# Kernel tuning notes

Hardware: AMD Instinct MI355X
Metric: run time of the kernel (lower is better)

The kernel has to match this reference:

```python
import jax, jax.numpy as jnp
import numpy as np
import math

C = 512
GROUPS = 32
EPS = 1e-06


def group_norm(x, w, b):
    # x: [B, C, H, W]; 32 groups over channels
    B, Cc, H, W = x.shape
    xg = x.reshape(B, GROUPS, Cc // GROUPS, H, W)
    mu = jnp.mean(xg, axis=(2, 3, 4), keepdims=True)
    var = jnp.var(xg, axis=(2, 3, 4), keepdims=True)
    xn = ((xg - mu) * jax.lax.rsqrt(var + EPS)).reshape(B, Cc, H, W)
    return xn * w[None, :, None, None] + b[None, :, None, None]


def setup_inputs() -> dict:
    key = jax.random.key(0)
    ks = jax.random.split(key, 7)
    B, H, W = 2, 64, 64
    x = jax.random.normal(ks[0], (B, C, H, W), dtype=jnp.float32)
    gn_w = jnp.ones((C,), dtype=jnp.float32)
    gn_b = jnp.zeros((C,), dtype=jnp.float32)
    s = 1.0 / math.sqrt(C)
    qkv_w = jax.random.normal(ks[1], (3 * C, C), dtype=jnp.float32) * s
    qkv_b = jnp.zeros((3 * C,), dtype=jnp.float32)
    proj_w = jax.random.normal(ks[2], (C, C), dtype=jnp.float32) * s
    proj_b = jnp.zeros((C,), dtype=jnp.float32)
    return {"x": x, "gn_w": gn_w, "gn_b": gn_b, "qkv_w": qkv_w,
            "qkv_b": qkv_b, "proj_w": proj_w, "proj_b": proj_b}


def reference(x, gn_w, gn_b, qkv_w, qkv_b, proj_w, proj_b):
    residue = x
    B, Cc, H, W = x.shape
    N = H * W
    constant = 1.0 / math.sqrt(Cc)
    xn = group_norm(x, gn_w, gn_b)
    # 1x1 conv == channel matmul
    qkv = jnp.einsum('bchw,oc->bohw', xn, qkv_w) + qkv_b[None, :, None, None]
    q, k, v = jnp.split(qkv, 3, axis=1)
    q = q.reshape(B, Cc, N)
    k = k.reshape(B, Cc, N)
    v = v.reshape(B, Cc, N)
    # attn[b,i,j] = sum_c k[b,c,i] * q[b,c,j]   (k^T @ q, per original code)
    attn = jnp.einsum('bci,bcj->bij', k, q) * constant
    soft = jax.nn.softmax(attn, axis=2)  # softmax over q-index j, as in torch dim=2
    # output[b,c,i] = sum_j v[b,c,j] * soft[b,j,i]   (v @ soft)
    out = jnp.einsum('bcj,bji->bci', v, soft).reshape(B, Cc, H, W)
    proj = jnp.einsum('bchw,oc->bohw', out, proj_w) + proj_b[None, :, None, None]
    return residue + proj
```

## Files before the change

kernel.cpp:

```cpp
#include <hip/hip_runtime.h>
#include <hip/hip_bf16.h>
#include <math.h>

typedef unsigned short ushort_t;
typedef __attribute__((ext_vector_type(8))) unsigned short ushort8;
typedef __attribute__((ext_vector_type(8))) __bf16 bf16x8;
typedef __attribute__((ext_vector_type(4))) float f32x4;

__device__ inline ushort_t f2b(float f) {
  __hip_bfloat16 h = __float2bfloat16(f);
  return __builtin_bit_cast(ushort_t, h);
}
__device__ inline float b2f(ushort_t u) {
  __hip_bfloat16 h = __builtin_bit_cast(__hip_bfloat16, u);
  return __bfloat162float(h);
}

__device__ inline void gload16(const ushort_t* g, ushort_t* l) {
  __builtin_amdgcn_global_load_lds(
      (const __attribute__((address_space(1))) unsigned int*)g,
      (__attribute__((address_space(3))) unsigned int*)l, 16, 0, 0);
}

__device__ inline void xcd_swz(int& bx, int& by, int& bz) {
  const int nx = gridDim.x, ny = gridDim.y;
  const int nwg = nx * ny * gridDim.z;
  const int orig = blockIdx.x + nx * (blockIdx.y + ny * blockIdx.z);
  const int q = nwg >> 3, r = nwg & 7, xcd = orig & 7, loc = orig >> 3;
  const int wg = (xcd < r ? xcd * (q + 1) : r * (q + 1) + (xcd - r) * q) + loc;
  bx = wg % nx;
  by = (wg / nx) % ny;
  bz = wg / (nx * ny);
}

__global__ __launch_bounds__(256) void prep_weights(
    const float* __restrict__ qkv_w, const float* __restrict__ proj_w,
    ushort_t* __restrict__ qkvw, ushort_t* __restrict__ projw) {
  int idx = blockIdx.x * 256 + threadIdx.x;
  const int NQ = 1536 * 512;
  if (idx < NQ) {
    qkvw[idx] = f2b(qkv_w[idx]);
  } else {
    int j = idx - NQ;
    if (j < 512 * 512) projw[j] = f2b(proj_w[j]);
  }
}

__global__ __launch_bounds__(256) void gn_stats(const float* __restrict__ x,
                                                float* __restrict__ stats) {
  const int tid = threadIdx.x;
  const int bg = blockIdx.x;
  const float4* xv = (const float4*)(x + (size_t)bg * 65536);
  float s = 0.f, ss = 0.f;
  for (int i = tid; i < 16384; i += 256) {
    float4 v = xv[i];
    s += v.x + v.y + v.z + v.w;
    ss += v.x * v.x + v.y * v.y + v.z * v.z + v.w * v.w;
  }
  __shared__ float red[8];
  for (int off = 32; off > 0; off >>= 1) {
    s += __shfl_down(s, off);
    ss += __shfl_down(ss, off);
  }
  if ((tid & 63) == 0) { red[tid >> 6] = s; red[4 + (tid >> 6)] = ss; }
  __syncthreads();
  if (tid == 0) {
    float st = red[0] + red[1] + red[2] + red[3];
    float sst = red[4] + red[5] + red[6] + red[7];
    float mean = st * (1.f / 65536.f);
    float var = sst * (1.f / 65536.f) - mean * mean;
    stats[bg * 2] = mean;
    stats[bg * 2 + 1] = rsqrtf(var + 1e-6f);
  }
}

__global__ __launch_bounds__(256) void gn_apply_t(
    const float* __restrict__ x, const float* __restrict__ w,
    const float* __restrict__ bgn, const float* __restrict__ stats,
    ushort_t* __restrict__ xnT) {
  __shared__ ushort_t tile[64][68];
  const int b = blockIdx.z;
  const int p0 = blockIdx.x * 64, c0 = blockIdx.y * 64;
  const int tid = threadIdx.x;
  const float* xb = x + ((size_t)b * 512 + c0) * 4096 + p0;
  const int tc = tid >> 4, tp = (tid & 15) * 4;
#pragma unroll
  for (int pass = 0; pass < 4; ++pass) {
    int c = pass * 16 + tc;
    int cg = c0 + c;
    float mean = stats[(b * 32 + (cg >> 4)) * 2];
    float inv = stats[(b * 32 + (cg >> 4)) * 2 + 1];
    float wc = w[cg] * inv;
    float bc = bgn[cg] - mean * wc;
    float4 v = *(const float4*)(xb + (size_t)c * 4096 + tp);
    tile[c][tp] = f2b(v.x * wc + bc);
    tile[c][tp + 1] = f2b(v.y * wc + bc);
    tile[c][tp + 2] = f2b(v.z * wc + bc);
    tile[c][tp + 3] = f2b(v.w * wc + bc);
  }
  __syncthreads();
  const int c8 = (tid & 7) * 8;
#pragma unroll
  for (int pass = 0; pass < 2; ++pass) {
    int p = pass * 32 + (tid >> 3);
    ushort8 u;
#pragma unroll
    for (int e = 0; e < 8; ++e) u[e] = tile[c8 + e][p];
    *(ushort8*)(xnT + ((size_t)b * 4096 + p0 + p) * 512 + c0 + c8) = u;
  }
}

template <int EPI>
__global__ __launch_bounds__(512, 2) void gemm8(
    const ushort_t* __restrict__ A, const ushort_t* __restrict__ B,
    void* __restrict__ Cg, const float* __restrict__ bias,
    float* __restrict__ smp, int N, int K, int lda, int ldb, size_t sA,
    size_t sB, size_t sC, float scale) {
  __shared__ __align__(16) ushort_t Al[2][256 * 64];
  __shared__ __align__(16) ushort_t Bl[2][256 * 64];
  __shared__ float s_max[2][256], s_sum[2][256];

  int bx, by, bz;
  xcd_swz(bx, by, bz);
  const ushort_t* Ab = A + bz * sA;
  const ushort_t* Bb = B + bz * sB;
  const int bm0 = by * 256, bn0 = bx * 256;
  const int tid = threadIdx.x;
  const int w = tid >> 6, lane = tid & 63;
  const int wr = w >> 2, wc = w & 3;
  const int fr = lane & 15, fq = lane >> 4;

  const int srow = tid >> 3, scb = tid & 7;
  const int ssw = scb ^ (srow & 7);
  const ushort_t* aS = Ab + (size_t)(bm0 + srow) * lda + ssw * 8;
  const ushort_t* bS = Bb + (size_t)(bn0 + srow) * ldb + ssw * 8;

  auto stage_a = [&](int s, int kk) {
#pragma unroll
    for (int g = 0; g < 4; ++g)
      gload16(aS + (size_t)(g * 64) * lda + kk, &Al[s][g * 4096 + w * 512]);
  };
  auto stage_b = [&](int s, int kk) {
#pragma unroll
    for (int g = 0; g < 4; ++g)
      gload16(bS + (size_t)(g * 64) * ldb + kk, &Bl[s][g * 4096 + w * 512]);
  };

  f32x4 acc[8][4] = {};
  bf16x8 a_r[4][2], b_r[4][2];

  auto read_a = [&](int s, int mh) {
#pragma unroll
    for (int mi = 0; mi < 4; ++mi) {
      int row = wr * 128 + mh * 64 + mi * 16 + fr;
#pragma unroll
      for (int ks = 0; ks < 2; ++ks) {
        int blk = ((ks * 4 + fq) ^ (row & 7)) * 8;
        a_r[mi][ks] = *(const bf16x8*)&Al[s][row * 64 + blk];
      }
    }
  };
  auto read_b = [&](int s, int nh) {
#pragma unroll
    for (int ni = 0; ni < 2; ++ni) {
      int row = wc * 64 + nh * 32 + ni * 16 + fr;
#pragma unroll
      for (int ks = 0; ks < 2; ++ks) {
        int blk = ((ks * 4 + fq) ^ (row & 7)) * 8;
        b_r[nh * 2 + ni][ks] = *(const bf16x8*)&Bl[s][row * 64 + blk];
      }
    }
  };
  auto phase_mfma = [&](int mh, int nh) {
    __builtin_amdgcn_s_setprio(1);
#pragma unroll
    for (int ks = 0; ks < 2; ++ks)
#pragma unroll
      for (int mi = 0; mi < 4; ++mi)
#pragma unroll
        for (int ni = 0; ni < 2; ++ni)
          acc[mh * 4 + mi][nh * 2 + ni] =
              __builtin_amdgcn_mfma_f32_16x16x32_bf16(
                  a_r[mi][ks], b_r[nh * 2 + ni][ks],
                  acc[mh * 4 + mi][nh * 2 + ni], 0, 0, 0);
    __builtin_amdgcn_s_setprio(0);
  };

  const int nt = K >> 6;
  stage_b(0, 0);
  stage_a(0, 0);
  if (nt > 1) {
    stage_b(1, 64);
    stage_a(1, 64);
    asm volatile("s_waitcnt vmcnt(8)" ::: "memory");
  } else {
    asm volatile("s_waitcnt vmcnt(0)" ::: "memory");
  }
  __builtin_amdgcn_s_barrier();

  for (int t = 0; t < nt; ++t) {
    const int s = t & 1;
    const int kk2 = (t + 2) << 6;
    const bool st2 = (t + 2) < nt;
    read_a(s, 0);
    read_b(s, 0);
    __builtin_amdgcn_s_barrier();
    phase_mfma(0, 0);
    __builtin_amdgcn_s_barrier();
    read_b(s, 1);
    __builtin_amdgcn_s_barrier();
    phase_mfma(0, 1);
    __builtin_amdgcn_s_barrier();
    read_a(s, 1);
    asm volatile("" ::: "memory");
    if (st2) stage_b(s, kk2);
    __builtin_amdgcn_s_barrier();
    phase_mfma(1, 0);
    __builtin_amdgcn_s_barrier();
    asm volatile("" ::: "memory");
    if (st2) stage_a(s, kk2);
    __builtin_amdgcn_s_barrier();
    phase_mfma(1, 1);
    if (st2)
      asm volatile("s_waitcnt vmcnt(8)" ::: "memory");
    else if (t + 1 < nt)
      asm volatile("s_waitcnt vmcnt(0)" ::: "memory");
    __builtin_amdgcn_s_barrier();
  }

  const size_t cbase = (size_t)bz * sC;
#pragma unroll
  for (int mi = 0; mi < 8; ++mi) {
#pragma unroll
    for (int r = 0; r < 4; ++r) {
      int gm = bm0 + wr * 128 + mi * 16 + fq * 4 + r;
#pragma unroll
      for (int ni = 0; ni < 4; ++ni) {
        int gn = bn0 + wc * 64 + ni * 16 + fr;
        float v = acc[mi][ni][r];
        size_t off = cbase + (size_t)gm * N + gn;
        ((ushort_t*)Cg)[off] = f2b(__expf(fminf(v * scale, 80.f)));
      }
    }
  }

  if constexpr (EPI == 2) {
    float cm[4], cs4[4];
#pragma unroll
    for (int ni = 0; ni < 4; ++ni) {
      float m = -3e38f;
#pragma unroll
      for (int mi = 0; mi < 8; ++mi)
#pragma unroll
        for (int r = 0; r < 4; ++r) m = fmaxf(m, acc[mi][ni][r] * scale);
      m = fmaxf(m, __shfl_xor(m, 16));
      m = fmaxf(m, __shfl_xor(m, 32));
      float s = 0.f;
#pragma unroll
      for (int mi = 0; mi < 8; ++mi)
#pragma unroll
        for (int r = 0; r < 4; ++r) s += __expf(acc[mi][ni][r] * scale - m);
      s += __shfl_xor(s, 16);
      s += __shfl_xor(s, 32);
      cm[ni] = m;
      cs4[ni] = s;
    }
    __syncthreads();
    if (lane < 16) {
#pragma unroll
      for (int ni = 0; ni < 4; ++ni) {
        s_max[wr][wc * 64 + ni * 16 + lane] = cm[ni];
        s_sum[wr][wc * 64 + ni * 16 + lane] = cs4[ni];
      }
    }
    __syncthreads();
    if (tid < 256) {
      float m0 = s_max[0][tid], m1 = s_max[1][tid];
      float M = fmaxf(m0, m1);
      float S = s_sum[0][tid] * __expf(m0 - M) + s_sum[1][tid] * __expf(m1 - M);
      size_t o = (((size_t)bz * 16 + by) * 4096 + bn0 + tid) * 2;
      smp[o] = M;
      smp[o + 1] = S;
    }
  }
}

template <int EPI>
__global__ __launch_bounds__(256) void gemm_pl(
    const ushort_t* __restrict__ A, const ushort_t* __restrict__ B,
    void* __restrict__ Cg, const float* __restrict__ bias,
    const float* __restrict__ colsc, int N, int K, int lda, int ldb,
    size_t sA, size_t sB, size_t sC) {
  __shared__ __align__(16) ushort_t Al[2][128 * 64];
  __shared__ __align__(16) ushort_t Bl[2][128 * 64];
  int bx, by, bz;
  xcd_swz(bx, by, bz);
  const ushort_t* Ab = A + bz * sA;
  const ushort_t* Bb = B + bz * sB;
  const int bm0 = by * 128, bn0 = bx * 128;
  const int tid = threadIdx.x;
  const int w = tid >> 6, lane = tid & 63;
  const int wm = (w >> 1) * 64, wn = (w & 1) * 64;
  const int fr = lane & 15, fq = lane >> 4;

  const int srow = tid >> 3, scb = tid & 7;
  const int ssw = scb ^ (srow & 7);
  const ushort_t* aS = Ab + (size_t)(bm0 + srow) * lda + ssw * 8;
  const ushort_t* bS = Bb + (size_t)(bn0 + srow) * ldb + ssw * 8;

  auto stage = [&](int s, int kk) {
#pragma unroll
    for (int g = 0; g < 4; ++g)
      gload16(aS + (size_t)(g * 32) * lda + kk, &Al[s][g * 2048 + w * 512]);
#pragma unroll
    for (int g = 0; g < 4; ++g)
      gload16(bS + (size_t)(g * 32) * ldb + kk, &Bl[s][g * 2048 + w * 512]);
  };

  f32x4 acc[4][4] = {};
  bf16x8 a_r[4][2], b_r[4][2];

  const int nt = K >> 6;
  stage(0, 0);
  if (nt > 1) {
    stage(1, 64);
    asm volatile("s_waitcnt vmcnt(8)" ::: "memory");
  } else {
    asm volatile("s_waitcnt vmcnt(0)" ::: "memory");
  }
  __builtin_amdgcn_s_barrier();

  for (int t = 0; t < nt; ++t) {
    const int s = t & 1;
#pragma unroll
    for (int mi = 0; mi < 4; ++mi) {
      int row = wm + mi * 16 + fr;
#pragma unroll
      for (int ks = 0; ks < 2; ++ks) {
        int blk = ((ks * 4 + fq) ^ (row & 7)) * 8;
        a_r[mi][ks] = *(const bf16x8*)&Al[s][row * 64 + blk];
      }
    }
#pragma unroll
    for (int ni = 0; ni < 4; ++ni) {
      int row = wn + ni * 16 + fr;
#pragma unroll
      for (int ks = 0; ks < 2; ++ks) {
        int blk = ((ks * 4 + fq) ^ (row & 7)) * 8;
        b_r[ni][ks] = *(const bf16x8*)&Bl[s][row * 64 + blk];
      }
    }
    __builtin_amdgcn_s_barrier();
    __builtin_amdgcn_s_setprio(1);
#pragma unroll
    for (int ks = 0; ks < 2; ++ks)
#pragma unroll
      for (int mi = 0; mi < 4; ++mi)
#pragma unroll
        for (int ni = 0; ni < 2; ++ni)
          acc[mi][ni] = __builtin_amdgcn_mfma_f32_16x16x32_bf16(
              a_r[mi][ks], b_r[ni][ks], acc[mi][ni], 0, 0, 0);
    __builtin_amdgcn_s_setprio(0);
    __builtin_amdgcn_s_barrier();
    if (t + 2 < nt) stage(s, (t + 2) << 6);
    __builtin_amdgcn_s_setprio(1);
#pragma unroll
    for (int ks = 0; ks < 2; ++ks)
#pragma unroll
      for (int mi = 0; mi < 4; ++mi)
#pragma unroll
        for (int ni = 2; ni < 4; ++ni)
          acc[mi][ni] = __builtin_amdgcn_mfma_f32_16x16x32_bf16(
              a_r[mi][ks], b_r[ni][ks], acc[mi][ni], 0, 0, 0);
    __builtin_amdgcn_s_setprio(0);
    if (t + 2 < nt)
      asm volatile("s_waitcnt vmcnt(8)" ::: "memory");
    else if (t + 1 < nt)
      asm volatile("s_waitcnt vmcnt(0)" ::: "memory");
    __builtin_amdgcn_s_barrier();
  }

  const int r0 = (lane >> 4) * 4;
  const size_t cbase = (size_t)bz * sC;
#pragma unroll
  for (int mi = 0; mi < 4; mi++) {
#pragma unroll
    for (int r = 0; r < 4; r++) {
      int gm = bm0 + wm + mi * 16 + r0 + r;
#pragma unroll
      for (int ni = 0; ni < 4; ni++) {
        int gn = bn0 + wn + ni * 16 + fr;
        float v = acc[mi][ni][r];
        size_t off = cbase + (size_t)gm * N + gn;
        if constexpr (EPI == 0) {
          ((ushort_t*)Cg)[off] = f2b(v + bias[gn]);
        } else if constexpr (EPI == 3) {
          ((ushort_t*)Cg)[off] = f2b(v * colsc[(size_t)bz * 4096 + gn]);
        } else {
          ((ushort_t*)Cg)[off] = f2b(v);
        }
      }
    }
  }
}

__global__ __launch_bounds__(256) void sm_fin(const float* __restrict__ part,
                                              float* __restrict__ alpha) {
  int idx = blockIdx.x * 256 + threadIdx.x;
  int b = idx >> 12, j = idx & 4095;
  float M = -3e38f, S = 0.f;
#pragma unroll
  for (int rc = 0; rc < 16; rc++) {
    size_t o = (((size_t)b * 16 + rc) * 4096 + j) * 2;
    float mi = part[o], si = part[o + 1];
    float nm = fmaxf(M, mi);
    S = S * __expf(M - nm) + si * __expf(mi - nm);
    M = nm;
  }
  alpha[idx] = __expf(-M) / S;
}

__global__ __launch_bounds__(256) void finalize(
    const ushort_t* __restrict__ outT, const float* __restrict__ x,
    const float* __restrict__ pb, float* __restrict__ out) {
  __shared__ ushort_t tile[64][72];
  const int b = blockIdx.z;
  const int p0 = blockIdx.x * 64, o0 = blockIdx.y * 64;
  const int tid = threadIdx.x;
  const int tp = tid >> 2, to = (tid & 3) * 16;
  const ushort8* src =
      (const ushort8*)(outT + ((size_t)b * 4096 + p0 + tp) * 512 + o0 + to);
  ushort8 u0 = src[0], u1 = src[1];
  *(ushort8*)&tile[tp][to] = u0;
  *(ushort8*)&tile[tp][to + 8] = u1;
  __syncthreads();
  const int wo = tid >> 2, wp = (tid & 3) * 16;
  float bias = pb[o0 + wo];
  const float* xr = x + ((size_t)b * 512 + o0 + wo) * 4096 + p0 + wp;
  float* orow = out + ((size_t)b * 512 + o0 + wo) * 4096 + p0 + wp;
#pragma unroll
  for (int e = 0; e < 16; ++e)
    orow[e] = b2f(tile[wp + e][wo]) + xr[e] + bias;
}

extern "C" void kernel_launch(void* const* d_in, const int* in_sizes, int n_in,
                              void* d_out, int out_size, void* d_ws,
                              size_t ws_size, hipStream_t stream) {
  const float* x = (const float*)d_in[0];
  const float* gn_w = (const float*)d_in[1];
  const float* gn_b = (const float*)d_in[2];
  const float* qkv_w = (const float*)d_in[3];
  const float* qkv_b = (const float*)d_in[4];
  const float* proj_w = (const float*)d_in[5];
  const float* proj_b = (const float*)d_in[6];
  float* out = (float*)d_out;

  char* ws = (char*)d_ws;
  ushort_t* xnT   = (ushort_t*)(ws);
  ushort_t* Wpp   = (ushort_t*)(ws);
  ushort_t* qkvw  = (ushort_t*)(ws + 8388608);
  ushort_t* projw = (ushort_t*)(ws + 9961472);
  float*    stats = (float*)(ws + 10485760);
  ushort_t* qkvT  = (ushort_t*)(ws + 10486272);
  ushort_t* outT  = (ushort_t*)(ws + 10486272);
  ushort_t* P     = (ushort_t*)(ws + 35652096);
  float*    smp   = (float*)(ws + 102760960);
  float*    alpha = (float*)(ws + 104858112);

  const float scale = 0.04419417382415922f;
  const size_t sXN = 2097152, sQKV = (size_t)4096 * 1536, sP = 16777216;

  prep_weights<<<4096, 256, 0, stream>>>(qkv_w, proj_w, qkvw, projw);
  gn_stats<<<64, 256, 0, stream>>>(x, stats);
  gn_apply_t<<<dim3(64, 8, 2), 256, 0, stream>>>(x, gn_w, gn_b, stats, xnT);
  gemm_pl<0><<<dim3(12, 64, 1), 256, 0, stream>>>(
      xnT, qkvw, qkvT, qkv_b, nullptr, 1536, 512, 512, 512, 0, 0, 0);
  gemm8<2><<<dim3(16, 16, 2), 512, 0, stream>>>(
      qkvT, qkvT + 512, P, nullptr, smp, 4096, 512, 1536, 1536, sQKV, sQKV,
      sP, scale);
  sm_fin<<<32, 256, 0, stream>>>(smp, alpha);
  gemm_pl<3><<<dim3(32, 4, 2), 256, 0, stream>>>(
      projw, qkvT + 1024, Wpp, nullptr, alpha, 4096, 512, 512, 1536, 0, sQKV,
      sXN);
  gemm_pl<5><<<dim3(4, 32, 2), 256, 0, stream>>>(
      P, Wpp, outT, nullptr, nullptr, 512, 4096, 4096, 4096, sP, sXN, sXN);
  finalize<<<dim3(64, 8, 2), 256, 0, stream>>>(outT, x, proj_b, out);
}
```

Measured before the change: 190.4 us.

## Split-K the final P×Wpp GEMM into two halves and reduce in finalize

The last GEMM (K=4096, only 256 blocks) is split along K into two halves, doubling the grid to 512 blocks. Each half writes a bf16 partial result, and the finalize kernel sums the two partials in fp32 before the transpose and residual add. The aim is better occupancy of the 256 CUs on a long-K GEMM with a small output. The cost is an extra partial-result buffer write and read, plus an extra bf16 rounding of each partial. Launch bounds are also changed to request 2 blocks per CU.

```diff
diff --git a/kernel.cpp b/kernel.cpp
--- a/kernel.cpp
+++ b/kernel.cpp
@@ -285,18 +285,19 @@
   }
 }
 
-template <int EPI>
-__global__ __launch_bounds__(256) void gemm_pl(
+template <int EPI, int SPLIT>
+__global__ __launch_bounds__(256, 2) void gemm_pl(
     const ushort_t* __restrict__ A, const ushort_t* __restrict__ B,
     void* __restrict__ Cg, const float* __restrict__ bias,
     const float* __restrict__ colsc, int N, int K, int lda, int ldb,
-    size_t sA, size_t sB, size_t sC) {
+    size_t sA, size_t sB, size_t sC, size_t sSp) {
   __shared__ __align__(16) ushort_t Al[2][128 * 64];
   __shared__ __align__(16) ushort_t Bl[2][128 * 64];
-  int bx, by, bz;
-  xcd_swz(bx, by, bz);
-  const ushort_t* Ab = A + bz * sA;
-  const ushort_t* Bb = B + bz * sB;
+  int bx, by, bzt;
+  xcd_swz(bx, by, bzt);
+  const int bz = bzt / SPLIT, sp = bzt % SPLIT;
+  const ushort_t* Ab = A + bz * sA + (size_t)sp * K;
+  const ushort_t* Bb = B + bz * sB + (size_t)sp * K;
   const int bm0 = by * 128, bn0 = bx * 128;
   const int tid = threadIdx.x;
   const int w = tid >> 6, lane = tid & 63;
@@ -381,7 +382,7 @@
   }
 
   const int r0 = (lane >> 4) * 4;
-  const size_t cbase = (size_t)bz * sC;
+  const size_t cbase = (size_t)sp * sSp + (size_t)bz * sC;
 #pragma unroll
   for (int mi = 0; mi < 4; mi++) {
 #pragma unroll
@@ -421,18 +422,23 @@
 }
 
 __global__ __launch_bounds__(256) void finalize(
-    const ushort_t* __restrict__ outT, const float* __restrict__ x,
+    const ushort_t* __restrict__ part, const float* __restrict__ x,
     const float* __restrict__ pb, float* __restrict__ out) {
-  __shared__ ushort_t tile[64][72];
+  __shared__ float tile[64][68];
   const int b = blockIdx.z;
   const int p0 = blockIdx.x * 64, o0 = blockIdx.y * 64;
   const int tid = threadIdx.x;
   const int tp = tid >> 2, to = (tid & 3) * 16;
-  const ushort8* src =
-      (const ushort8*)(outT + ((size_t)b * 4096 + p0 + tp) * 512 + o0 + to);
-  ushort8 u0 = src[0], u1 = src[1];
-  *(ushort8*)&tile[tp][to] = u0;
-  *(ushort8*)&tile[tp][to + 8] = u1;
+  const size_t base = ((size_t)b * 4096 + p0 + tp) * 512 + o0 + to;
+  ushort8 u0 = *(const ushort8*)(part + base);
+  ushort8 u1 = *(const ushort8*)(part + base + 8);
+  ushort8 v0 = *(const ushort8*)(part + 4194304 + base);
+  ushort8 v1 = *(const ushort8*)(part + 4194304 + base + 8);
+#pragma unroll
+  for (int e = 0; e < 8; ++e) {
+    tile[tp][to + e] = b2f(u0[e]) + b2f(v0[e]);
+    tile[tp][to + 8 + e] = b2f(u1[e]) + b2f(v1[e]);
+  }
   __syncthreads();
   const int wo = tid >> 2, wp = (tid & 3) * 16;
   float bias = pb[o0 + wo];
@@ -440,7 +446,7 @@
   float* orow = out + ((size_t)b * 512 + o0 + wo) * 4096 + p0 + wp;
 #pragma unroll
   for (int e = 0; e < 16; ++e)
-    orow[e] = b2f(tile[wp + e][wo]) + xr[e] + bias;
+    orow[e] = tile[wp + e][wo] + xr[e] + bias;
 }
 
 extern "C" void kernel_launch(void* const* d_in, const int* in_sizes, int n_in,
@@ -462,7 +468,7 @@
   ushort_t* projw = (ushort_t*)(ws + 9961472);
   float*    stats = (float*)(ws + 10485760);
   ushort_t* qkvT  = (ushort_t*)(ws + 10486272);
-  ushort_t* outT  = (ushort_t*)(ws + 10486272);
+  ushort_t* part  = (ushort_t*)(ws + 10486272);
   ushort_t* P     = (ushort_t*)(ws + 35652096);
   float*    smp   = (float*)(ws + 102760960);
   float*    alpha = (float*)(ws + 104858112);
@@ -473,16 +479,17 @@
   prep_weights<<<4096, 256, 0, stream>>>(qkv_w, proj_w, qkvw, projw);
   gn_stats<<<64, 256, 0, stream>>>(x, stats);
   gn_apply_t<<<dim3(64, 8, 2), 256, 0, stream>>>(x, gn_w, gn_b, stats, xnT);
-  gemm_pl<0><<<dim3(12, 64, 1), 256, 0, stream>>>(
-      xnT, qkvw, qkvT, qkv_b, nullptr, 1536, 512, 512, 512, 0, 0, 0);
+  gemm_pl<0, 1><<<dim3(12, 64, 1), 256, 0, stream>>>(
+      xnT, qkvw, qkvT, qkv_b, nullptr, 1536, 512, 512, 512, 0, 0, 0, 0);
   gemm8<2><<<dim3(16, 16, 2), 512, 0, stream>>>(
       qkvT, qkvT + 512, P, nullptr, smp, 4096, 512, 1536, 1536, sQKV, sQKV,
       sP, scale);
   sm_fin<<<32, 256, 0, stream>>>(smp, alpha);
-  gemm_pl<3><<<dim3(32, 4, 2), 256, 0, stream>>>(
+  gemm_pl<3, 1><<<dim3(32, 4, 2), 256, 0, stream>>>(
       projw, qkvT + 1024, Wpp, nullptr, alpha, 4096, 512, 512, 1536, 0, sQKV,
-      sXN);
-  gemm_pl<5><<<dim3(4, 32, 2), 256, 0, stream>>>(
-      P, Wpp, outT, nullptr, nullptr, 512, 4096, 4096, 4096, sP, sXN, sXN);
-  finalize<<<dim3(64, 8, 2), 256, 0, stream>>>(outT, x, proj_b, out);
-}
+      sXN, 0);
+  gemm_pl<5, 2><<<dim3(4, 32, 4), 256, 0, stream>>>(
+      P, Wpp, part, nullptr, nullptr, 512, 2048, 4096, 4096, sP, sXN, sXN,
+      4194304);
+  finalize<<<dim3(64, 8, 2), 256, 0, stream>>>(part, x, proj_b, out);
+}
```

Result: faster. 171.7 us (-9.8%).
